# Optimization experiments

Measured on AMD Instinct MI355X. Metric: run time of the kernel, lower is better.

Reference implementation:

```python
import jax, jax.numpy as jnp
import numpy as np

N = 100000
E = 1600000
DIN = 165
DH = 128


def setup_inputs() -> dict:
    key = jax.random.key(0)
    ks = jax.random.split(key, 10)
    def nrm(k, shape, scale=0.1):
        return jax.random.normal(k, shape, dtype=jnp.float32) * scale
    x = jax.random.normal(ks[0], (N, DIN), dtype=jnp.float32)
    edge_index = jax.random.randint(ks[1], (2, E), 0, N, dtype=jnp.int64)
    return dict(
        x=x,
        edge_index=edge_index,
        fb_w1=nrm(ks[2], (DIN, DIN // 2)),
        fb_w2=nrm(ks[3], (DIN // 2, DIN)),
        sage_wl=nrm(ks[4], (DIN, DH)),
        sage_bl=jnp.zeros((DH,), jnp.float32),
        sage_wr=nrm(ks[5], (DIN, DH)),
        gat_w=nrm(ks[6], (DH, DH // 2)),
        gat_att_src=nrm(ks[7], (DH // 2,)),
        gat_att_dst=nrm(ks[8], (DH // 2,)),
        gat_b=jnp.zeros((DH // 2,), jnp.float32),
        cheb_w=nrm(ks[9], (DH // 2, 1)),
        cheb_b=jnp.zeros((1,), jnp.float32),
    )


def _segment_softmax(logits, seg, num_segments):
    mx = jax.ops.segment_max(logits, seg, num_segments=num_segments)
    e = jnp.exp(logits - mx[seg])
    s = jax.ops.segment_sum(e, seg, num_segments=num_segments)
    return e / (s[seg] + 1e-16)


def reference(x, edge_index, fb_w1, fb_w2, sage_wl, sage_bl, sage_wr,
              gat_w, gat_att_src, gat_att_dst, gat_b, cheb_w, cheb_b):
    n = x.shape[0]
    src, dst = edge_index[0], edge_index[1]

    # FeatureBooster: scatter over batch=arange(n) is identity for max and sum,
    # so max_result == sum_result == x and y = sigmoid(mlp(x) + mlp(x)).
    m = jnp.maximum(x @ fb_w1, 0.0) @ fb_w2
    x = x * jax.nn.sigmoid(m + m)

    # SAGEConv (mean aggregation): out = lin_l(mean_agg(x_src -> dst)) + lin_r(x)
    agg = jax.ops.segment_sum(x[src], dst, num_segments=n)  # [n, DIN]
    cnt = jax.ops.segment_sum(jnp.ones((src.shape[0],), x.dtype), dst, num_segments=n)
    agg = agg / jnp.maximum(cnt, 1.0)[:, None]
    x = agg @ sage_wl + sage_bl + x @ sage_wr
    x = jnp.maximum(x, 0.0)  # relu; dropout is identity in eval mode

    # GATConv (heads=1) with default add_self_loops=True
    ar = jnp.arange(n, dtype=src.dtype)
    si = jnp.concatenate([src, ar])
    di = jnp.concatenate([dst, ar])
    h = x @ gat_w                      # [n, 64]
    a_s = h @ gat_att_src              # [n]
    a_d = h @ gat_att_dst              # [n]
    e = a_s[si] + a_d[di]
    e = jnp.where(e > 0, e, 0.2 * e)   # leaky_relu slope 0.2
    alpha = _segment_softmax(e, di, n)
    x = jax.ops.segment_sum(h[si] * alpha[:, None], di, num_segments=n) + gat_b
    x = jnp.maximum(x, 0.0)

    # ChebConv with K=1: T_0(x) = x, so it's a plain linear layer.
    x = x @ cheb_w + cheb_b
    return jax.nn.sigmoid(x)
```

## Files before the change

kernel.cpp:

```cpp
#include <hip/hip_runtime.h>
#include <hip/hip_bf16.h>

#define N_NODES 100000
#define N_EDGES 1600000
#define EHALF 800000
#define DIN 165
#define DHID 82
#define DH 128
#define DG 64
#define XPS 168
#define HS 88
#define SLOTS 60

typedef _Float16 f16;
typedef f16 f16x8 __attribute__((ext_vector_type(8)));
typedef f16 f16x4 __attribute__((ext_vector_type(4)));
typedef float f32x4 __attribute__((ext_vector_type(4)));

#define MFMA16(a, b, c) __builtin_amdgcn_mfma_f32_16x16x32_f16(a, b, c, 0, 0, 0)


__global__ __launch_bounds__(256) void xpad_kernel(const float* __restrict__ x,
                                                   f16* __restrict__ Xp) {
    int gid = blockIdx.x * 256 + threadIdx.x;
    if (gid >= N_NODES * 42) return;
    int node = gid / 42, g = gid % 42;
    int col0 = g * 4;
    f16x4 o;
#pragma unroll
    for (int j = 0; j < 4; j++) {
        int c = col0 + j;
        o[j] = (f16)((c < DIN) ? x[(long)node * DIN + c] : 0.f);
    }
    *((f16x4*)(Xp + (long)node * XPS + col0)) = o;
}

__global__ __launch_bounds__(256) void h_fill_kernel(const f16* __restrict__ Xp,
                                                     const float* __restrict__ w1,
                                                     f16* __restrict__ H,
                                                     const int* __restrict__ dst,
                                                     const int* __restrict__ src,
                                                     int* __restrict__ cnt,
                                                     int* __restrict__ slots) {
    int tid = threadIdx.x, wave = tid >> 6, lane = tid & 63;
    {
        int tg = blockIdx.x * 256 + tid;
        for (int e = tg; e < EHALF; e += 384 * 256) {
            int d = dst[e];
            int r = atomicAdd(&cnt[d], 1);
            if (r < SLOTS) slots[(long)d * SLOTS + r] = src[e];
        }
    }
    int q = lane >> 4, l16 = lane & 15;
    int blk = blockIdx.x;
    int g = (blk >> 3) & 1;
    int chunk = (blk & 7) + 8 * (blk >> 4);
    int nbase = g * 48;
    f16x8 bf[3][6];
#pragma unroll
    for (int nt = 0; nt < 3; nt++) {
        int col = nbase + nt * 16 + l16;
#pragma unroll
        for (int ks = 0; ks < 6; ks++) {
            int kb = ks * 32 + q * 8;
            f16x8 b;
#pragma unroll
            for (int j = 0; j < 8; j++) {
                int k = kb + j;
                b[j] = (f16)((k < DIN && col < DHID) ? w1[k * DHID + col] : 0.f);
            }
            bf[nt][ks] = b;
        }
    }
    for (int mt = chunk * 4 + wave; mt < 6250; mt += 768) {
        const f16* xr = Xp + (long)(mt * 16 + l16) * XPS;
        f32x4 acc[3];
#pragma unroll
        for (int nt = 0; nt < 3; nt++) acc[nt] = (f32x4){0.f, 0.f, 0.f, 0.f};
#pragma unroll
        for (int ks = 0; ks < 6; ks++) {
            f16x8 a = *((const f16x8*)(xr + ks * 32 + q * 8));
#pragma unroll
            for (int nt = 0; nt < 3; nt++) acc[nt] = MFMA16(a, bf[nt][ks], acc[nt]);
        }
#pragma unroll
        for (int nt = 0; nt < 3; nt++) {
            int col = nbase + nt * 16 + l16;
            if (col < HS) {
#pragma unroll
                for (int r = 0; r < 4; r++) {
                    int node = mt * 16 + q * 4 + r;
                    H[(long)node * HS + col] = (f16)fmaxf(acc[nt][r], 0.f);
                }
            }
        }
    }
}

__global__ __launch_bounds__(256) void y_kernel(const f16* __restrict__ Xp,
                                                const f16* __restrict__ H,
                                                const float* __restrict__ w2,
                                                f16* __restrict__ Y,
                                                const int* __restrict__ dst,
                                                const int* __restrict__ src,
                                                int* __restrict__ cnt,
                                                int* __restrict__ slots) {
    int tid = threadIdx.x, wave = tid >> 6, lane = tid & 63;
    {
        int tg = blockIdx.x * 256 + tid;
        for (int e = EHALF + tg; e < N_EDGES; e += 768 * 256) {
            int d = dst[e];
            int r = atomicAdd(&cnt[d], 1);
            if (r < SLOTS) slots[(long)d * SLOTS + r] = src[e];
        }
    }
    int q = lane >> 4, l16 = lane & 15;
    int blk = blockIdx.x;
    int g = (blk >> 3) & 3;
    int chunk = (blk & 7) + 8 * (blk >> 5);
    int nbase = g * 48;
    f16x8 bf[3][3];
#pragma unroll
    for (int nt = 0; nt < 3; nt++) {
        int col = nbase + nt * 16 + l16;
#pragma unroll
        for (int ks = 0; ks < 3; ks++) {
            int kb = ks * 32 + q * 8;
            f16x8 b;
#pragma unroll
            for (int j = 0; j < 8; j++) {
                int k = kb + j;
                b[j] = (f16)((k < DHID && col < DIN) ? w2[k * DIN + col] : 0.f);
            }
            bf[nt][ks] = b;
        }
    }
    for (int mt = chunk * 4 + wave; mt < 6250; mt += 768) {
        const f16* hr = H + (long)(mt * 16 + l16) * HS;
        f32x4 acc[3];
#pragma unroll
        for (int nt = 0; nt < 3; nt++) acc[nt] = (f32x4){0.f, 0.f, 0.f, 0.f};
#pragma unroll
        for (int ks = 0; ks < 3; ks++) {
            f16x8 a = *((const f16x8*)(hr + ks * 32 + q * 8));
#pragma unroll
            for (int nt = 0; nt < 3; nt++) acc[nt] = MFMA16(a, bf[nt][ks], acc[nt]);
        }
#pragma unroll
        for (int nt = 0; nt < 3; nt++) {
            int col = nbase + nt * 16 + l16;
            if (col < XPS) {
#pragma unroll
                for (int r = 0; r < 4; r++) {
                    int node = mt * 16 + q * 4 + r;
                    float gg = 1.f / (1.f + __expf(-2.f * acc[nt][r]));
                    float xv = (float)Xp[(long)node * XPS + col];
                    Y[(long)node * XPS + col] = (f16)(xv * gg);
                }
            }
        }
    }
}

__global__ __launch_bounds__(256) void sage_lin_kernel(const f16* __restrict__ Y,
                                                       const float* __restrict__ wl,
                                                       const float* __restrict__ wr,
                                                       const float* __restrict__ bl,
                                                       f16* __restrict__ t_l,
                                                       f16* __restrict__ x2) {
    int tid = threadIdx.x, wave = tid >> 6, lane = tid & 63;
    int q = lane >> 4, l16 = lane & 15;
    int blk = blockIdx.x;
    int g = (blk >> 3) & 3;
    int chunk = (blk & 7) + 8 * (blk >> 5);
    bool isR = (g >= 2);
    const float* W = isR ? wr : wl;
    int cbase = (g & 1) * 64;
    f16x8 bf[4][6];
    float blv[4];
#pragma unroll
    for (int nt = 0; nt < 4; nt++) {
        int col = cbase + nt * 16 + l16;
        blv[nt] = isR ? bl[col] : 0.f;
#pragma unroll
        for (int ks = 0; ks < 6; ks++) {
            int kb = ks * 32 + q * 8;
            f16x8 b;
#pragma unroll
            for (int j = 0; j < 8; j++) {
                int k = kb + j;
                b[j] = (f16)((k < DIN) ? W[k * DH + col] : 0.f);
            }
            bf[nt][ks] = b;
        }
    }
    for (int mt = chunk * 4 + wave; mt < 6250; mt += 768) {
        const f16* yrow = Y + (long)(mt * 16 + l16) * XPS;
        f32x4 acc[4];
#pragma unroll
        for (int nt = 0; nt < 4; nt++) acc[nt] = (f32x4){0.f, 0.f, 0.f, 0.f};
#pragma unroll
        for (int ks = 0; ks < 6; ks++) {
            f16x8 a = *((const f16x8*)(yrow + ks * 32 + q * 8));
#pragma unroll
            for (int nt = 0; nt < 4; nt++) acc[nt] = MFMA16(a, bf[nt][ks], acc[nt]);
        }
#pragma unroll
        for (int nt = 0; nt < 4; nt++) {
            int col = cbase + nt * 16 + l16;
#pragma unroll
            for (int r = 0; r < 4; r++) {
                int node = mt * 16 + q * 4 + r;
                if (isR)
                    x2[(long)node * DH + col] = (f16)(acc[nt][r] + blv[nt]);
                else
                    t_l[(long)node * DH + col] = (f16)acc[nt][r];
            }
        }
    }
}

__global__ __launch_bounds__(256) void sage_agg_kernel(const f16* __restrict__ t_l,
                                                       const int* __restrict__ cnt,
                                                       const int* __restrict__ slots,
                                                       f16* __restrict__ x2) {
    int wid = threadIdx.x >> 6, lane = threadIdx.x & 63;
    int i = blockIdx.x * 4 + wid;
    int deg = cnt[i];
    int quarter = lane >> 4, fq = lane & 15;
    float acc[8];
#pragma unroll
    for (int k = 0; k < 8; k++) acc[k] = 0.f;
    int sn_v = (lane < deg) ? slots[(long)i * SLOTS + lane] : 0;
    int jmax = (deg + 3) >> 2;
    for (int j = 0; j < jmax; j++) {
        int idx = 4 * j + quarter;
        int sn = __shfl(sn_v, idx);
        float v = (idx < deg) ? 1.f : 0.f;
        f16x8 p = *((const f16x8*)(t_l + ((long)sn << 7) + fq * 8));
#pragma unroll
        for (int k = 0; k < 8; k++) acc[k] = fmaf(v, (float)p[k], acc[k]);
    }
#pragma unroll
    for (int k = 0; k < 8; k++) {
        acc[k] += __shfl_xor(acc[k], 16);
        acc[k] += __shfl_xor(acc[k], 32);
    }
    if (quarter == 0) {
        float inv = 1.f / fmaxf((float)deg, 1.f);
        f16x8* xp = (f16x8*)(x2 + (long)i * DH + fq * 8);
        f16x8 pre = *xp;
        f16x8 o;
#pragma unroll
        for (int k = 0; k < 8; k++) o[k] = (f16)fmaxf((float)pre[k] + acc[k] * inv, 0.f);
        *xp = o;
    }
}

__global__ __launch_bounds__(256) void gat_h_kernel(const f16* __restrict__ x2,
                                                    const float* __restrict__ gw,
                                                    const float* __restrict__ att_s_w,
                                                    const float* __restrict__ att_d_w,
                                                    f16* __restrict__ h,
                                                    float* __restrict__ a_s,
                                                    float* __restrict__ a_d) {
    int tid = threadIdx.x, wave = tid >> 6, lane = tid & 63;
    int q = lane >> 4, l16 = lane & 15;
    f16x8 bf[4][4];
    float asw[4], adw[4];
#pragma unroll
    for (int nt = 0; nt < 4; nt++) {
        int col = nt * 16 + l16;
        asw[nt] = att_s_w[col];
        adw[nt] = att_d_w[col];
#pragma unroll
        for (int ks = 0; ks < 4; ks++) {
            int kb = ks * 32 + q * 8;
            f16x8 b;
#pragma unroll
            for (int j = 0; j < 8; j++) b[j] = (f16)gw[(kb + j) * DG + col];
            bf[nt][ks] = b;
        }
    }
    int stride = gridDim.x * 4;
    for (int mt = blockIdx.x * 4 + wave; mt < 6250; mt += stride) {
        const f16* xr = x2 + (long)(mt * 16 + l16) * DH;
        f32x4 acc[4];
#pragma unroll
        for (int nt = 0; nt < 4; nt++) acc[nt] = (f32x4){0.f, 0.f, 0.f, 0.f};
#pragma unroll
        for (int ks = 0; ks < 4; ks++) {
            f16x8 a = *((const f16x8*)(xr + ks * 32 + q * 8));
#pragma unroll
            for (int nt = 0; nt < 4; nt++) acc[nt] = MFMA16(a, bf[nt][ks], acc[nt]);
        }
#pragma unroll
        for (int r = 0; r < 4; r++) {
            int node = mt * 16 + q * 4 + r;
            float vs = 0.f, vd = 0.f;
#pragma unroll
            for (int nt = 0; nt < 4; nt++) {
                float hv = acc[nt][r];
                h[(long)node * DG + nt * 16 + l16] = (f16)hv;
                vs += hv * asw[nt];
                vd += hv * adw[nt];
            }
#pragma unroll
            for (int off = 1; off < 16; off <<= 1) {
                vs += __shfl_xor(vs, off);
                vd += __shfl_xor(vd, off);
            }
            if (l16 == 0) {
                a_s[node] = vs;
                a_d[node] = vd;
            }
        }
    }
}

__device__ __forceinline__ float leaky02(float v) { return v > 0.f ? v : 0.2f * v; }

__global__ __launch_bounds__(256) void gat_agg_kernel(const f16* __restrict__ h,
                                                      const float* __restrict__ a_s,
                                                      const float* __restrict__ a_d,
                                                      const int* __restrict__ cnt,
                                                      const int* __restrict__ slots,
                                                      const float* __restrict__ gat_b,
                                                      const float* __restrict__ cheb_w,
                                                      const float* __restrict__ cheb_b,
                                                      float* __restrict__ out) {
    int wid = threadIdx.x >> 6, lane = threadIdx.x & 63;
    int i = blockIdx.x * 4 + wid;
    int deg = cnt[i];
    int quarter = lane >> 4, fq = lane & 15;
    float adi = a_d[i];
    float acc[4] = {0.f, 0.f, 0.f, 0.f};
    int sn_v = (lane < deg) ? slots[(long)i * SLOTS + lane] : 0;
    float ev = 0.f;
    if (lane < deg) ev = __expf(leaky02(a_s[sn_v] + adi));
    float sv = ev;
    int jmax = (deg + 3) >> 2;
    for (int j = 0; j < jmax; j++) {
        int idx = 4 * j + quarter;
        int sn = __shfl(sn_v, idx);
        float w = __shfl(ev, idx);
        f16x4 p = *((const f16x4*)(h + ((long)sn << 6) + fq * 4));
#pragma unroll
        for (int k = 0; k < 4; k++) acc[k] = fmaf(w, (float)p[k], acc[k]);
    }
#pragma unroll
    for (int off = 32; off > 0; off >>= 1) sv += __shfl_xor(sv, off);
#pragma unroll
    for (int k = 0; k < 4; k++) {
        acc[k] += __shfl_xor(acc[k], 16);
        acc[k] += __shfl_xor(acc[k], 32);
    }
    if (quarter == 0) {
        float wself = __expf(leaky02(a_s[i] + adi));
        float s = sv + wself;
        f16x4 ph = *((const f16x4*)(h + ((long)i << 6) + fq * 4));
        float4 gb = ((const float4*)gat_b)[fq];
        float4 cw = ((const float4*)cheb_w)[fq];
        float gbv[4] = {gb.x, gb.y, gb.z, gb.w};
        float cwv[4] = {cw.x, cw.y, cw.z, cw.w};
        float inv = 1.f / s;
        float z = 0.f;
#pragma unroll
        for (int k = 0; k < 4; k++) {
            float o = fmaxf(fmaf(wself, (float)ph[k], acc[k]) * inv + gbv[k], 0.f);
            z = fmaf(o, cwv[k], z);
        }
#pragma unroll
        for (int off = 8; off > 0; off >>= 1) z += __shfl_xor(z, off);
        if (fq == 0) out[i] = 1.f / (1.f + __expf(-(z + cheb_b[0])));
    }
}

extern "C" void kernel_launch(void* const* d_in, const int* in_sizes, int n_in,
                              void* d_out, int out_size, void* d_ws, size_t ws_size,
                              hipStream_t stream) {
    const float* x       = (const float*)d_in[0];
    const int*   eidx    = (const int*)d_in[1];
    const float* fb_w1   = (const float*)d_in[2];
    const float* fb_w2   = (const float*)d_in[3];
    const float* sage_wl = (const float*)d_in[4];
    const float* sage_bl = (const float*)d_in[5];
    const float* sage_wr = (const float*)d_in[6];
    const float* gat_w   = (const float*)d_in[7];
    const float* att_src = (const float*)d_in[8];
    const float* att_dst = (const float*)d_in[9];
    const float* gat_b   = (const float*)d_in[10];
    const float* cheb_w  = (const float*)d_in[11];
    const float* cheb_b  = (const float*)d_in[12];

    const int* src = eidx;
    const int* dst = eidx + N_EDGES;

    char* base = (char*)d_ws;
    f16* Xp  = (f16*)base;
    f16* H   = (f16*)(base + 33600000);
    f16* Y   = (f16*)(base + 51200000);
    f16* t_l = (f16*)base;
    f16* x2  = (f16*)(base + 25600000);
    f16* h   = (f16*)(base + 51200000);
    float* a_s = (float*)(base + 64000000);
    float* a_d = a_s + N_NODES;
    int* cnt   = (int*)(base + 84800000);
    int* slots = (int*)(base + 85200000);

    hipMemsetAsync(cnt, 0, N_NODES * sizeof(int), stream);

    xpad_kernel<<<(N_NODES * 42 + 255) / 256, 256, 0, stream>>>(x, Xp);
    h_fill_kernel<<<384, 256, 0, stream>>>(Xp, fb_w1, H, dst, src, cnt, slots);
    y_kernel<<<768, 256, 0, stream>>>(Xp, H, fb_w2, Y, dst, src, cnt, slots);
    sage_lin_kernel<<<768, 256, 0, stream>>>(Y, sage_wl, sage_wr, sage_bl, t_l, x2);
    sage_agg_kernel<<<N_NODES / 4, 256, 0, stream>>>(t_l, cnt, slots, x2);
    gat_h_kernel<<<392, 256, 0, stream>>>(x2, gat_w, att_src, att_dst, h, a_s, a_d);
    gat_agg_kernel<<<N_NODES / 4, 256, 0, stream>>>(h, a_s, a_d, cnt, slots, gat_b,
                                                    cheb_w, cheb_b, (float*)d_out);
}
```

Baseline: 470.1 us.

## Spread edge bucketing across four kernels using dedicated scatter blocks

Edge slot-filling moves out of the compute blocks' prologue. It is split into four quarters, each handled by 96 extra blocks launched alongside xpad, h_fill, y and sage_lin. These scatter blocks run concurrently with the dense MFMA/elementwise blocks instead of delaying every compute block. The cost is extra blocks per launch and block-index remapping, and atomic traffic now overlaps with memory-bound work.

```diff
diff --git a/kernel.cpp b/kernel.cpp
--- a/kernel.cpp
+++ b/kernel.cpp
@@ -3,7 +3,7 @@
 
 #define N_NODES 100000
 #define N_EDGES 1600000
-#define EHALF 800000
+#define EQ 400000
 #define DIN 165
 #define DHID 82
 #define DH 128
@@ -11,6 +11,7 @@
 #define XPS 168
 #define HS 88
 #define SLOTS 60
+#define SCB 96
 
 typedef _Float16 f16;
 typedef f16 f16x8 __attribute__((ext_vector_type(8)));
@@ -20,9 +21,29 @@
 #define MFMA16(a, b, c) __builtin_amdgcn_mfma_f32_16x16x32_f16(a, b, c, 0, 0, 0)
 
 
+__device__ __forceinline__ void scatter_edges(int e0, int e1, int tg,
+                                              const int* __restrict__ dst,
+                                              const int* __restrict__ src,
+                                              int* __restrict__ cnt,
+                                              int* __restrict__ slots) {
+    for (int e = e0 + tg; e < e1; e += SCB * 256) {
+        int d = dst[e];
+        int r = atomicAdd(&cnt[d], 1);
+        if (r < SLOTS) slots[(long)d * SLOTS + r] = src[e];
+    }
+}
+
 __global__ __launch_bounds__(256) void xpad_kernel(const float* __restrict__ x,
-                                                   f16* __restrict__ Xp) {
-    int gid = blockIdx.x * 256 + threadIdx.x;
+                                                   f16* __restrict__ Xp,
+                                                   const int* __restrict__ dst,
+                                                   const int* __restrict__ src,
+                                                   int* __restrict__ cnt,
+                                                   int* __restrict__ slots) {
+    if (blockIdx.x < SCB) {
+        scatter_edges(0, EQ, blockIdx.x * 256 + threadIdx.x, dst, src, cnt, slots);
+        return;
+    }
+    int gid = (blockIdx.x - SCB) * 256 + threadIdx.x;
     if (gid >= N_NODES * 42) return;
     int node = gid / 42, g = gid % 42;
     int col0 = g * 4;
@@ -43,16 +64,12 @@
                                                      int* __restrict__ cnt,
                                                      int* __restrict__ slots) {
     int tid = threadIdx.x, wave = tid >> 6, lane = tid & 63;
-    {
-        int tg = blockIdx.x * 256 + tid;
-        for (int e = tg; e < EHALF; e += 384 * 256) {
-            int d = dst[e];
-            int r = atomicAdd(&cnt[d], 1);
-            if (r < SLOTS) slots[(long)d * SLOTS + r] = src[e];
-        }
+    if (blockIdx.x < SCB) {
+        scatter_edges(EQ, 2 * EQ, blockIdx.x * 256 + tid, dst, src, cnt, slots);
+        return;
     }
     int q = lane >> 4, l16 = lane & 15;
-    int blk = blockIdx.x;
+    int blk = blockIdx.x - SCB;
     int g = (blk >> 3) & 1;
     int chunk = (blk & 7) + 8 * (blk >> 4);
     int nbase = g * 48;
@@ -106,16 +123,12 @@
                                                 int* __restrict__ cnt,
                                                 int* __restrict__ slots) {
     int tid = threadIdx.x, wave = tid >> 6, lane = tid & 63;
-    {
-        int tg = blockIdx.x * 256 + tid;
-        for (int e = EHALF + tg; e < N_EDGES; e += 768 * 256) {
-            int d = dst[e];
-            int r = atomicAdd(&cnt[d], 1);
-            if (r < SLOTS) slots[(long)d * SLOTS + r] = src[e];
-        }
+    if (blockIdx.x < SCB) {
+        scatter_edges(2 * EQ, 3 * EQ, blockIdx.x * 256 + tid, dst, src, cnt, slots);
+        return;
     }
     int q = lane >> 4, l16 = lane & 15;
-    int blk = blockIdx.x;
+    int blk = blockIdx.x - SCB;
     int g = (blk >> 3) & 3;
     int chunk = (blk & 7) + 8 * (blk >> 5);
     int nbase = g * 48;
@@ -167,10 +180,18 @@
                                                        const float* __restrict__ wr,
                                                        const float* __restrict__ bl,
                                                        f16* __restrict__ t_l,
-                                                       f16* __restrict__ x2) {
+                                                       f16* __restrict__ x2,
+                                                       const int* __restrict__ dst,
+                                                       const int* __restrict__ src,
+                                                       int* __restrict__ cnt,
+                                                       int* __restrict__ slots) {
     int tid = threadIdx.x, wave = tid >> 6, lane = tid & 63;
+    if (blockIdx.x < SCB) {
+        scatter_edges(3 * EQ, N_EDGES, blockIdx.x * 256 + tid, dst, src, cnt, slots);
+        return;
+    }
     int q = lane >> 4, l16 = lane & 15;
-    int blk = blockIdx.x;
+    int blk = blockIdx.x - SCB;
     int g = (blk >> 3) & 3;
     int chunk = (blk & 7) + 8 * (blk >> 5);
     bool isR = (g >= 2);
@@ -410,10 +431,12 @@
 
     hipMemsetAsync(cnt, 0, N_NODES * sizeof(int), stream);
 
-    xpad_kernel<<<(N_NODES * 42 + 255) / 256, 256, 0, stream>>>(x, Xp);
-    h_fill_kernel<<<384, 256, 0, stream>>>(Xp, fb_w1, H, dst, src, cnt, slots);
-    y_kernel<<<768, 256, 0, stream>>>(Xp, H, fb_w2, Y, dst, src, cnt, slots);
-    sage_lin_kernel<<<768, 256, 0, stream>>>(Y, sage_wl, sage_wr, sage_bl, t_l, x2);
+    xpad_kernel<<<SCB + (N_NODES * 42 + 255) / 256, 256, 0, stream>>>(
+        x, Xp, dst, src, cnt, slots);
+    h_fill_kernel<<<SCB + 384, 256, 0, stream>>>(Xp, fb_w1, H, dst, src, cnt, slots);
+    y_kernel<<<SCB + 768, 256, 0, stream>>>(Xp, H, fb_w2, Y, dst, src, cnt, slots);
+    sage_lin_kernel<<<SCB + 768, 256, 0, stream>>>(Y, sage_wl, sage_wr, sage_bl,
+                                                   t_l, x2, dst, src, cnt, slots);
     sage_agg_kernel<<<N_NODES / 4, 256, 0, stream>>>(t_l, cnt, slots, x2);
     gat_h_kernel<<<392, 256, 0, stream>>>(x2, gat_w, att_src, att_dst, h, a_s, a_d);
     gat_agg_kernel<<<N_NODES / 4, 256, 0, stream>>>(h, a_s, a_d, cnt, slots, gat_b,
```

After: 456.3 us. 1.03x faster.

## Move edge scatter into xpad kernel and double GEMM grid sizes

Applied to the files above, without the earlier changes.

Edge bucketing (atomic counts plus slot writes) moves out of the two feature-booster GEMM kernels into extra blocks of the xpad kernel, so the MFMA kernels no longer carry atomic scatter work. The GEMM kernels are launched with twice the blocks and a matching tile stride to raise occupancy. The aggregation kernels clamp degree to the slot capacity, hoist the self-row and parameter loads ahead of the neighbor loop, and unroll that loop. Running the scatter alongside the memory-bound xpad conversion may contend for bandwidth.

```diff
diff --git a/kernel.cpp b/kernel.cpp
--- a/kernel.cpp
+++ b/kernel.cpp
@@ -3,7 +3,6 @@
 
 #define N_NODES 100000
 #define N_EDGES 1600000
-#define EHALF 800000
 #define DIN 165
 #define DHID 82
 #define DH 128
@@ -11,6 +10,7 @@
 #define XPS 168
 #define HS 88
 #define SLOTS 60
+#define SCBX 2048
 
 typedef _Float16 f16;
 typedef f16 f16x8 __attribute__((ext_vector_type(8)));
@@ -20,9 +20,30 @@
 #define MFMA16(a, b, c) __builtin_amdgcn_mfma_f32_16x16x32_f16(a, b, c, 0, 0, 0)
 
 
+__device__ __forceinline__ void scatter_edges(int tg,
+                                              const int* __restrict__ dst,
+                                              const int* __restrict__ src,
+                                              int* __restrict__ cnt,
+                                              int* __restrict__ slots) {
+#pragma unroll 4
+    for (int e = tg; e < N_EDGES; e += SCBX * 256) {
+        int d = dst[e];
+        int r = atomicAdd(&cnt[d], 1);
+        if (r < SLOTS) slots[(long)d * SLOTS + r] = src[e];
+    }
+}
+
 __global__ __launch_bounds__(256) void xpad_kernel(const float* __restrict__ x,
-                                                   f16* __restrict__ Xp) {
-    int gid = blockIdx.x * 256 + threadIdx.x;
+                                                   f16* __restrict__ Xp,
+                                                   const int* __restrict__ dst,
+                                                   const int* __restrict__ src,
+                                                   int* __restrict__ cnt,
+                                                   int* __restrict__ slots) {
+    if (blockIdx.x < SCBX) {
+        scatter_edges(blockIdx.x * 256 + threadIdx.x, dst, src, cnt, slots);
+        return;
+    }
+    int gid = (blockIdx.x - SCBX) * 256 + threadIdx.x;
     if (gid >= N_NODES * 42) return;
     int node = gid / 42, g = gid % 42;
     int col0 = g * 4;
@@ -37,20 +58,8 @@
 
 __global__ __launch_bounds__(256) void h_fill_kernel(const f16* __restrict__ Xp,
                                                      const float* __restrict__ w1,
-                                                     f16* __restrict__ H,
-                                                     const int* __restrict__ dst,
-                                                     const int* __restrict__ src,
-                                                     int* __restrict__ cnt,
-                                                     int* __restrict__ slots) {
+                                                     f16* __restrict__ H) {
     int tid = threadIdx.x, wave = tid >> 6, lane = tid & 63;
-    {
-        int tg = blockIdx.x * 256 + tid;
-        for (int e = tg; e < EHALF; e += 384 * 256) {
-            int d = dst[e];
-            int r = atomicAdd(&cnt[d], 1);
-            if (r < SLOTS) slots[(long)d * SLOTS + r] = src[e];
-        }
-    }
     int q = lane >> 4, l16 = lane & 15;
     int blk = blockIdx.x;
     int g = (blk >> 3) & 1;
@@ -72,7 +81,7 @@
             bf[nt][ks] = b;
         }
     }
-    for (int mt = chunk * 4 + wave; mt < 6250; mt += 768) {
+    for (int mt = chunk * 4 + wave; mt < 6250; mt += 1536) {
         const f16* xr = Xp + (long)(mt * 16 + l16) * XPS;
         f32x4 acc[3];
 #pragma unroll
@@ -100,20 +109,8 @@
 __global__ __launch_bounds__(256) void y_kernel(const f16* __restrict__ Xp,
                                                 const f16* __restrict__ H,
                                                 const float* __restrict__ w2,
-                                                f16* __restrict__ Y,
-                                                const int* __restrict__ dst,
-                                                const int* __restrict__ src,
-                                                int* __restrict__ cnt,
-                                                int* __restrict__ slots) {
+                                                f16* __restrict__ Y) {
     int tid = threadIdx.x, wave = tid >> 6, lane = tid & 63;
-    {
-        int tg = blockIdx.x * 256 + tid;
-        for (int e = EHALF + tg; e < N_EDGES; e += 768 * 256) {
-            int d = dst[e];
-            int r = atomicAdd(&cnt[d], 1);
-            if (r < SLOTS) slots[(long)d * SLOTS + r] = src[e];
-        }
-    }
     int q = lane >> 4, l16 = lane & 15;
     int blk = blockIdx.x;
     int g = (blk >> 3) & 3;
@@ -135,7 +132,7 @@
             bf[nt][ks] = b;
         }
     }
-    for (int mt = chunk * 4 + wave; mt < 6250; mt += 768) {
+    for (int mt = chunk * 4 + wave; mt < 6250; mt += 1536) {
         const f16* hr = H + (long)(mt * 16 + l16) * HS;
         f32x4 acc[3];
 #pragma unroll
@@ -194,7 +191,7 @@
             bf[nt][ks] = b;
         }
     }
-    for (int mt = chunk * 4 + wave; mt < 6250; mt += 768) {
+    for (int mt = chunk * 4 + wave; mt < 6250; mt += 1536) {
         const f16* yrow = Y + (long)(mt * 16 + l16) * XPS;
         f32x4 acc[4];
 #pragma unroll
@@ -226,13 +223,15 @@
                                                        f16* __restrict__ x2) {
     int wid = threadIdx.x >> 6, lane = threadIdx.x & 63;
     int i = blockIdx.x * 4 + wid;
-    int deg = cnt[i];
+    int deg = min(cnt[i], SLOTS);
     int quarter = lane >> 4, fq = lane & 15;
+    f16x8 pre = *((const f16x8*)(x2 + (long)i * DH + fq * 8));
     float acc[8];
 #pragma unroll
     for (int k = 0; k < 8; k++) acc[k] = 0.f;
     int sn_v = (lane < deg) ? slots[(long)i * SLOTS + lane] : 0;
     int jmax = (deg + 3) >> 2;
+#pragma unroll 4
     for (int j = 0; j < jmax; j++) {
         int idx = 4 * j + quarter;
         int sn = __shfl(sn_v, idx);
@@ -248,12 +247,10 @@
     }
     if (quarter == 0) {
         float inv = 1.f / fmaxf((float)deg, 1.f);
-        f16x8* xp = (f16x8*)(x2 + (long)i * DH + fq * 8);
-        f16x8 pre = *xp;
         f16x8 o;
 #pragma unroll
         for (int k = 0; k < 8; k++) o[k] = (f16)fmaxf((float)pre[k] + acc[k] * inv, 0.f);
-        *xp = o;
+        *((f16x8*)(x2 + (long)i * DH + fq * 8)) = o;
     }
 }
 
@@ -331,15 +328,20 @@
                                                       float* __restrict__ out) {
     int wid = threadIdx.x >> 6, lane = threadIdx.x & 63;
     int i = blockIdx.x * 4 + wid;
-    int deg = cnt[i];
+    int deg = min(cnt[i], SLOTS);
     int quarter = lane >> 4, fq = lane & 15;
     float adi = a_d[i];
+    f16x4 ph = *((const f16x4*)(h + ((long)i << 6) + fq * 4));
+    float4 gb = ((const float4*)gat_b)[fq];
+    float4 cw = ((const float4*)cheb_w)[fq];
+    float wself = __expf(leaky02(a_s[i] + adi));
     float acc[4] = {0.f, 0.f, 0.f, 0.f};
     int sn_v = (lane < deg) ? slots[(long)i * SLOTS + lane] : 0;
     float ev = 0.f;
     if (lane < deg) ev = __expf(leaky02(a_s[sn_v] + adi));
     float sv = ev;
     int jmax = (deg + 3) >> 2;
+#pragma unroll 4
     for (int j = 0; j < jmax; j++) {
         int idx = 4 * j + quarter;
         int sn = __shfl(sn_v, idx);
@@ -356,11 +358,7 @@
         acc[k] += __shfl_xor(acc[k], 32);
     }
     if (quarter == 0) {
-        float wself = __expf(leaky02(a_s[i] + adi));
         float s = sv + wself;
-        f16x4 ph = *((const f16x4*)(h + ((long)i << 6) + fq * 4));
-        float4 gb = ((const float4*)gat_b)[fq];
-        float4 cw = ((const float4*)cheb_w)[fq];
         float gbv[4] = {gb.x, gb.y, gb.z, gb.w};
         float cwv[4] = {cw.x, cw.y, cw.z, cw.w};
         float inv = 1.f / s;
@@ -410,10 +408,11 @@
 
     hipMemsetAsync(cnt, 0, N_NODES * sizeof(int), stream);
 
-    xpad_kernel<<<(N_NODES * 42 + 255) / 256, 256, 0, stream>>>(x, Xp);
-    h_fill_kernel<<<384, 256, 0, stream>>>(Xp, fb_w1, H, dst, src, cnt, slots);
-    y_kernel<<<768, 256, 0, stream>>>(Xp, H, fb_w2, Y, dst, src, cnt, slots);
-    sage_lin_kernel<<<768, 256, 0, stream>>>(Y, sage_wl, sage_wr, sage_bl, t_l, x2);
+    xpad_kernel<<<SCBX + (N_NODES * 42 + 255) / 256, 256, 0, stream>>>(
+        x, Xp, dst, src, cnt, slots);
+    h_fill_kernel<<<768, 256, 0, stream>>>(Xp, fb_w1, H);
+    y_kernel<<<1536, 256, 0, stream>>>(Xp, H, fb_w2, Y);
+    sage_lin_kernel<<<1536, 256, 0, stream>>>(Y, sage_wl, sage_wr, sage_bl, t_l, x2);
     sage_agg_kernel<<<N_NODES / 4, 256, 0, stream>>>(t_l, cnt, slots, x2);
     gat_h_kernel<<<392, 256, 0, stream>>>(x2, gat_w, att_src, att_dst, h, a_s, a_d);
     gat_agg_kernel<<<N_NODES / 4, 256, 0, stream>>>(h, a_s, a_d, cnt, slots, gat_b,
```

Measured after the change: 485.7 us. 1.03x slower.
